# Optimization experiments

Measured on AMD Instinct MI355X. Metric: run time of the kernel, lower is better.

The kernel has to match this reference:

```python
import jax, jax.numpy as jnp
import numpy as np

B, C, O = 16384, 128, 128


def setup_inputs() -> dict:
    key = jax.random.key(0)
    k1, k2, k3 = jax.random.split(key, 3)
    x = jax.random.normal(k1, (B, C, 3, 3), dtype=jnp.float32)
    # 9 stacked Conv2d(C, O, 3x3) weights/biases, position p = 3*r + c (row-major)
    W = jax.random.normal(k2, (9, O, C, 3, 3), dtype=jnp.float32) * 0.05
    b = jax.random.normal(k3, (9, O), dtype=jnp.float32) * 0.05
    return {"x": x, "W": W, "b": b}


def reference(x, W, b):
    Bn = x.shape[0]
    xr = x.reshape(Bn, C, 3, 3)
    # F.interpolate(scale_factor=3, mode='nearest'): each pixel replicated 3x3
    ins = jnp.repeat(jnp.repeat(xr, 3, axis=2), 3, axis=3)  # (B, C, 9, 9)
    # patch for output position (r, c) is ins[:, :, 2+r:5+r, 2+c:5+c]
    patches = jnp.stack(
        [ins[:, :, 2 + r:5 + r, 2 + c:5 + c] for r in range(3) for c in range(3)],
        axis=0,
    )  # (9, B, C, 3, 3)
    # each conv reduces its 3x3xC patch to one pixel per out-channel
    out = jnp.einsum('pbcij,pocij->bpo', patches, W) + b[None]  # (B, 9, O)
    out = out.transpose(0, 2, 1).reshape(Bn, O, 3, 3)  # row-major (r, c)
    return out
```

## Files before the change

kernel.cpp:

```cpp
#include <hip/hip_runtime.h>
#include <hip/hip_bf16.h>

typedef __bf16 bf16_t;
typedef __attribute__((ext_vector_type(8))) __bf16 bf16x8;
typedef __attribute__((ext_vector_type(4))) float f32x4;

#define KDIM 1152
#define NDIM 1152
#define BM 128
#define BN 192
#define BK 32
#define NIT 36
#define NTILES 6
#define A_STEP 8192
#define A_PANEL 294912
#define B_STEP 12288
#define B_TILE (36 * B_STEP)

__device__ __forceinline__ void gload_lds16(const void* g, void* l) {
    __builtin_amdgcn_global_load_lds(
        (const __attribute__((address_space(1))) void*)g,
        (__attribute__((address_space(3))) void*)l, 16, 0, 0);
}

__global__ void cvt_x(const float* __restrict__ X, bf16_t* __restrict__ Xb)
{
    const int u = blockIdx.x * 256 + threadIdx.x;
    const int w = u >> 9;
    const int P = w / 36;
    const int T = w - P * 36;
    const int rem = u & 511;
    const int rb = rem >> 6;
    const int g = (rem >> 4) & 3;
    const int r0 = rem & 15;
    const int m = P * 128 + rb * 16 + r0;
    const int k = T * 32 + g * 8;
    const float* src = X + (size_t)m * KDIM + k;
    f32x4 lo = *(const f32x4*)src;
    f32x4 hi = *(const f32x4*)(src + 4);
    bf16x8 v;
    #pragma unroll
    for (int e = 0; e < 4; ++e) { v[e] = (__bf16)lo[e]; v[4 + e] = (__bf16)hi[e]; }
    *(bf16x8*)((char*)Xb + (size_t)u * 16) = v;
}

__global__ void build_wb(const float* __restrict__ W,
                         const float* __restrict__ bvec,
                         bf16_t* __restrict__ Bm,
                         float* __restrict__ bias)
{
    const int t = blockIdx.x * blockDim.x + threadIdx.x;
    if (t < NDIM) {
        const int o = t / 9, p = t - o * 9;
        bias[t] = bvec[p * 128 + o];
    }
    const int c = t & 127;
    const int o = (t >> 7) & 127;
    const int p = t >> 14;
    if (p >= 9) return;
    const int r = p / 3, cc = p - r * 3;
    float eff[3][3] = {{0.f,0.f,0.f},{0.f,0.f,0.f},{0.f,0.f,0.f}};
    const float* w = W + (size_t)((p * 128 + o) * 128 + c) * 9;
    #pragma unroll
    for (int i = 0; i < 3; ++i) {
        const int a = (2 + r + i) / 3;
        #pragma unroll
        for (int j = 0; j < 3; ++j) {
            const int bb = (2 + cc + j) / 3;
            eff[a][bb] += w[i * 3 + j];
        }
    }
    const int n = o * 9 + p;
    const int tile = n / BN;
    const int nin = n - tile * BN;
    #pragma unroll
    for (int a = 0; a < 3; ++a)
        #pragma unroll
        for (int bb = 0; bb < 3; ++bb) {
            const int k = c * 9 + a * 3 + bb;
            const size_t idx = (size_t)tile * (B_TILE / 2)
                             + (k >> 5) * (B_STEP / 2)
                             + (nin >> 4) * 512 + ((k >> 3) & 3) * 128
                             + (nin & 15) * 8 + (k & 7);
            Bm[idx] = (bf16_t)eff[a][bb];
        }
}

__launch_bounds__(256, 3)
__global__ void ind_gemm(const bf16_t* __restrict__ Xb,
                         const bf16_t* __restrict__ Bm,
                         const float* __restrict__ bias,
                         float* __restrict__ out)
{
    __shared__ char As[2][A_STEP];
    __shared__ char Bs[2][B_STEP];

    const int tid = threadIdx.x;
    const int lane = tid & 63;
    const int wid = tid >> 6;
    const int wm = wid >> 1;
    const int wn = wid & 1;

    const int bid = blockIdx.x;
    const int swz = (bid & 7) * 96 + (bid >> 3);
    const int mt = swz / NTILES;
    const int nt = swz - mt * NTILES;
    const int m0 = mt * BM;

    const char* apanel = (const char*)Xb + (size_t)mt * A_PANEL;
    const char* bpanel = (const char*)Bm + (size_t)nt * B_TILE;
    const int fr = (lane >> 4) * 256 + (lane & 15) * 16;

    f32x4 acc[4][6];
    #pragma unroll
    for (int i = 0; i < 4; ++i)
        #pragma unroll
        for (int j = 0; j < 6; ++j)
            acc[i][j] = (f32x4){0.f, 0.f, 0.f, 0.f};

    #define GLDA(T, BUF) do {                                               \
        const char* s_ = apanel + (size_t)(T) * A_STEP;                     \
        gload_lds16(s_ + tid * 16,        &As[BUF][tid * 16]);              \
        gload_lds16(s_ + 4096 + tid * 16, &As[BUF][4096 + tid * 16]);       \
    } while (0)

    #define GLDB(T, BUF) do {                                               \
        const char* s_ = bpanel + (size_t)(T) * B_STEP;                     \
        _Pragma("unroll")                                                   \
        for (int r_ = 0; r_ < 3; ++r_) {                                    \
            const int u_ = (tid + r_ * 256) * 16;                           \
            gload_lds16(s_ + u_, &Bs[BUF][u_]);                             \
        } } while (0)

    GLDA(0, 0); GLDB(0, 0);
    GLDA(1, 1); GLDB(1, 1);
    asm volatile("s_waitcnt vmcnt(5)" ::: "memory");
    __builtin_amdgcn_sched_barrier(0);
    __builtin_amdgcn_s_barrier();

    #pragma unroll 1
    for (int t = 0; t < NIT; ++t) {
        const int cur = t & 1;
        bf16x8 af[4], bfr[6];
        #pragma unroll
        for (int mi = 0; mi < 4; ++mi)
            af[mi] = *(const bf16x8*)(&As[cur][(wm * 4 + mi) * 1024 + fr]);
        #pragma unroll
        for (int j = 0; j < 6; ++j)
            bfr[j] = *(const bf16x8*)(&Bs[cur][(wn * 6 + j) * 1024 + fr]);
        asm volatile("s_waitcnt lgkmcnt(0)" ::: "memory");
        __builtin_amdgcn_sched_barrier(0);
        __builtin_amdgcn_s_barrier();
        if (t < NIT - 2) {
            GLDA(t + 2, cur);
            GLDB(t + 2, cur);
        }
        __builtin_amdgcn_s_setprio(1);
        #pragma unroll
        for (int mi = 0; mi < 4; ++mi)
            #pragma unroll
            for (int j = 0; j < 6; ++j)
                acc[mi][j] = __builtin_amdgcn_mfma_f32_16x16x32_bf16(
                    af[mi], bfr[j], acc[mi][j], 0, 0, 0);
        __builtin_amdgcn_s_setprio(0);
        if (t < NIT - 2) {
            asm volatile("s_waitcnt vmcnt(5)" ::: "memory");
            __builtin_amdgcn_sched_barrier(0);
        } else if (t == NIT - 2) {
            asm volatile("s_waitcnt vmcnt(0)" ::: "memory");
            __builtin_amdgcn_sched_barrier(0);
        }
        if (t < NIT - 1) __builtin_amdgcn_s_barrier();
    }

    #undef GLDA
    #undef GLDB

    const int orow = (lane >> 4) * 4;
    const int ocol = lane & 15;
    const int gn0 = nt * BN + wn * 96 + ocol;
    #pragma unroll
    for (int ni = 0; ni < 6; ++ni) {
        const float bv = bias[gn0 + ni * 16];
        #pragma unroll
        for (int mi = 0; mi < 4; ++mi) {
            float* po = out + (size_t)(m0 + wm * 64 + mi * 16 + orow) * NDIM
                            + gn0 + ni * 16;
            #pragma unroll
            for (int r = 0; r < 4; ++r)
                po[(size_t)r * NDIM] = acc[mi][ni][r] + bv;
        }
    }
}

extern "C" void kernel_launch(void* const* d_in, const int* in_sizes, int n_in,
                              void* d_out, int out_size, void* d_ws, size_t ws_size,
                              hipStream_t stream)
{
    const float* x  = (const float*)d_in[0];
    const float* W  = (const float*)d_in[1];
    const float* bv = (const float*)d_in[2];
    float* out = (float*)d_out;

    bf16_t* Xb   = (bf16_t*)d_ws;
    bf16_t* Bm   = (bf16_t*)((char*)d_ws + (size_t)16384 * KDIM * sizeof(bf16_t));
    float*  bias = (float*)((char*)Bm + (size_t)KDIM * NDIM * sizeof(bf16_t));

    cvt_x<<<9216, 256, 0, stream>>>(x, Xb);
    build_wb<<<576, 256, 0, stream>>>(W, bv, Bm, bias);
    ind_gemm<<<768, 256, 0, stream>>>(Xb, Bm, bias, out);
}
```

Measured before the change: 89.44 us.

## Load A fragments directly from global into registers, bypassing LDS

The GEMM no longer stages the A panel in shared memory. Each wave loads its A fragments straight into VGPRs with inline-asm global_load_dwordx4, double-buffered in two register sets, and the loop is unrolled by two. Only B is staged through LDS now. This removes the A LDS traffic and its footprint, at the cost of more VGPRs and of duplicated global reads of A by the two wn waves.

```diff
diff --git a/kernel.cpp b/kernel.cpp
--- a/kernel.cpp
+++ b/kernel.cpp
@@ -92,7 +92,6 @@
                          const float* __restrict__ bias,
                          float* __restrict__ out)
 {
-    __shared__ char As[2][A_STEP];
     __shared__ char Bs[2][B_STEP];
 
     const int tid = threadIdx.x;
@@ -107,9 +106,9 @@
     const int nt = swz - mt * NTILES;
     const int m0 = mt * BM;
 
-    const char* apanel = (const char*)Xb + (size_t)mt * A_PANEL;
+    const int fr = (lane >> 4) * 256 + (lane & 15) * 16;
+    const char* apl = (const char*)Xb + (size_t)mt * A_PANEL + wm * 4096 + fr;
     const char* bpanel = (const char*)Bm + (size_t)nt * B_TILE;
-    const int fr = (lane >> 4) * 256 + (lane & 15) * 16;
 
     f32x4 acc[4][6];
     #pragma unroll
@@ -118,10 +117,16 @@
         for (int j = 0; j < 6; ++j)
             acc[i][j] = (f32x4){0.f, 0.f, 0.f, 0.f};
 
-    #define GLDA(T, BUF) do {                                               \
-        const char* s_ = apanel + (size_t)(T) * A_STEP;                     \
-        gload_lds16(s_ + tid * 16,        &As[BUF][tid * 16]);              \
-        gload_lds16(s_ + 4096 + tid * 16, &As[BUF][4096 + tid * 16]);       \
+    f32x4 afA[4], afB[4];
+
+    #define LOADA(T, AF) do {                                               \
+        const char* p_ = apl + (size_t)(T) * A_STEP;                        \
+        asm volatile("global_load_dwordx4 %0, %4, off\n\t"                  \
+                     "global_load_dwordx4 %1, %4, off offset:1024\n\t"      \
+                     "global_load_dwordx4 %2, %4, off offset:2048\n\t"      \
+                     "global_load_dwordx4 %3, %4, off offset:3072"          \
+                     : "=&v"(AF[0]), "=&v"(AF[1]), "=&v"(AF[2]), "=&v"(AF[3]) \
+                     : "v"(p_) : "memory");                                 \
     } while (0)
 
     #define GLDB(T, BUF) do {                                               \
@@ -132,49 +137,74 @@
             gload_lds16(s_ + u_, &Bs[BUF][u_]);                             \
         } } while (0)
 
-    GLDA(0, 0); GLDB(0, 0);
-    GLDA(1, 1); GLDB(1, 1);
-    asm volatile("s_waitcnt vmcnt(5)" ::: "memory");
+    #define MFMA24(AF) do {                                                 \
+        __builtin_amdgcn_s_setprio(1);                                      \
+        _Pragma("unroll")                                                   \
+        for (int mi = 0; mi < 4; ++mi) {                                    \
+            const bf16x8 a_ = __builtin_bit_cast(bf16x8, AF[mi]);           \
+            _Pragma("unroll")                                               \
+            for (int j_ = 0; j_ < 6; ++j_)                                  \
+                acc[mi][j_] = __builtin_amdgcn_mfma_f32_16x16x32_bf16(      \
+                    a_, bfr[j_], acc[mi][j_], 0, 0, 0);                     \
+        }                                                                   \
+        __builtin_amdgcn_s_setprio(0);                                      \
+    } while (0)
+
+    #define RDB(CUR) do {                                                   \
+        _Pragma("unroll")                                                   \
+        for (int j_ = 0; j_ < 6; ++j_)                                      \
+            bfr[j_] = *(const bf16x8*)(&Bs[CUR][(wn * 6 + j_) * 1024 + fr]); \
+        asm volatile("s_waitcnt lgkmcnt(0)" ::: "memory");                  \
+        __builtin_amdgcn_sched_barrier(0);                                  \
+        __builtin_amdgcn_s_barrier();                                       \
+    } while (0)
+
+    bf16x8 bfr[6];
+
+    LOADA(0, afA);
+    GLDB(0, 0);
+    GLDB(1, 1);
+    asm volatile("s_waitcnt vmcnt(3)" ::: "memory");
     __builtin_amdgcn_sched_barrier(0);
     __builtin_amdgcn_s_barrier();
 
     #pragma unroll 1
-    for (int t = 0; t < NIT; ++t) {
-        const int cur = t & 1;
-        bf16x8 af[4], bfr[6];
-        #pragma unroll
-        for (int mi = 0; mi < 4; ++mi)
-            af[mi] = *(const bf16x8*)(&As[cur][(wm * 4 + mi) * 1024 + fr]);
-        #pragma unroll
-        for (int j = 0; j < 6; ++j)
-            bfr[j] = *(const bf16x8*)(&Bs[cur][(wn * 6 + j) * 1024 + fr]);
+    for (int t2 = 0; t2 < 17; ++t2) {
+        const int t = 2 * t2;
+        RDB(0);
+        LOADA(t + 1, afB);
+        GLDB(t + 2, 0);
+        MFMA24(afA);
+        asm volatile("s_waitcnt vmcnt(3)" ::: "memory");
+        __builtin_amdgcn_sched_barrier(0);
+        __builtin_amdgcn_s_barrier();
+        RDB(1);
+        LOADA(t + 2, afA);
+        GLDB(t + 3, 1);
+        MFMA24(afB);
+        asm volatile("s_waitcnt vmcnt(3)" ::: "memory");
+        __builtin_amdgcn_sched_barrier(0);
+        __builtin_amdgcn_s_barrier();
+    }
+    RDB(0);
+    LOADA(35, afB);
+    MFMA24(afA);
+    asm volatile("s_waitcnt vmcnt(0)" ::: "memory");
+    __builtin_amdgcn_sched_barrier(0);
+    __builtin_amdgcn_s_barrier();
+    {
+        #pragma unroll
+        for (int j_ = 0; j_ < 6; ++j_)
+            bfr[j_] = *(const bf16x8*)(&Bs[1][(wn * 6 + j_) * 1024 + fr]);
         asm volatile("s_waitcnt lgkmcnt(0)" ::: "memory");
         __builtin_amdgcn_sched_barrier(0);
-        __builtin_amdgcn_s_barrier();
-        if (t < NIT - 2) {
-            GLDA(t + 2, cur);
-            GLDB(t + 2, cur);
-        }
-        __builtin_amdgcn_s_setprio(1);
-        #pragma unroll
-        for (int mi = 0; mi < 4; ++mi)
-            #pragma unroll
-            for (int j = 0; j < 6; ++j)
-                acc[mi][j] = __builtin_amdgcn_mfma_f32_16x16x32_bf16(
-                    af[mi], bfr[j], acc[mi][j], 0, 0, 0);
-        __builtin_amdgcn_s_setprio(0);
-        if (t < NIT - 2) {
-            asm volatile("s_waitcnt vmcnt(5)" ::: "memory");
-            __builtin_amdgcn_sched_barrier(0);
-        } else if (t == NIT - 2) {
-            asm volatile("s_waitcnt vmcnt(0)" ::: "memory");
-            __builtin_amdgcn_sched_barrier(0);
-        }
-        if (t < NIT - 1) __builtin_amdgcn_s_barrier();
-    }
-
-    #undef GLDA
+        MFMA24(afB);
+    }
+
+    #undef LOADA
     #undef GLDB
+    #undef MFMA24
+    #undef RDB
 
     const int orow = (lane >> 4) * 4;
     const int ocol = lane & 15;
```

Measured after the change: 90.53 us. Within noise of the previous version (+1.2%).

## Enlarge GEMM tiles to 256x288 with 512-thread blocks and 4-slot LDS ring

Applied to the files above, without the earlier changes.

The bf16 GEMM tile grows from 128x192 with 256 threads to 256x288 with 512 threads. The grid shrinks to 256 blocks, one per CU. Each block stages A and B into a 4-slot LDS ring, prefetching two steps ahead, and splits each K-step into two half-steps so global-to-LDS loads interleave with MFMA work. The aim is more data reuse per loaded byte and less global and L2 traffic. In exchange there are fewer resident waves per CU, higher register pressure from 36 accumulators per wave, and a scrap LDS write to keep the per-thread load count uniform.

```diff
diff --git a/kernel.cpp b/kernel.cpp
--- a/kernel.cpp
+++ b/kernel.cpp
@@ -7,15 +7,13 @@
 
 #define KDIM 1152
 #define NDIM 1152
-#define BM 128
-#define BN 192
-#define BK 32
-#define NIT 36
-#define NTILES 6
-#define A_STEP 8192
+#define BM 256
+#define BN 288
+#define NH 36
+#define NTILES 4
 #define A_PANEL 294912
-#define B_STEP 12288
-#define B_TILE (36 * B_STEP)
+#define B_SLAB 18432
+#define B_TILE (36 * B_SLAB)
 
 __device__ __forceinline__ void gload_lds16(const void* g, void* l) {
     __builtin_amdgcn_global_load_lds(
@@ -79,21 +77,22 @@
         for (int bb = 0; bb < 3; ++bb) {
             const int k = c * 9 + a * 3 + bb;
             const size_t idx = (size_t)tile * (B_TILE / 2)
-                             + (k >> 5) * (B_STEP / 2)
+                             + (k >> 5) * (B_SLAB / 2)
                              + (nin >> 4) * 512 + ((k >> 3) & 3) * 128
                              + (nin & 15) * 8 + (k & 7);
             Bm[idx] = (bf16_t)eff[a][bb];
         }
 }
 
-__launch_bounds__(256, 3)
+__launch_bounds__(512, 1)
 __global__ void ind_gemm(const bf16_t* __restrict__ Xb,
                          const bf16_t* __restrict__ Bm,
                          const float* __restrict__ bias,
                          float* __restrict__ out)
 {
-    __shared__ char As[2][A_STEP];
-    __shared__ char Bs[2][B_STEP];
+    __shared__ char Ar[4][16384];
+    __shared__ char Br[4][18432];
+    __shared__ char Scrap[1024];
 
     const int tid = threadIdx.x;
     const int lane = tid & 63;
@@ -102,85 +101,113 @@
     const int wn = wid & 1;
 
     const int bid = blockIdx.x;
-    const int swz = (bid & 7) * 96 + (bid >> 3);
-    const int mt = swz / NTILES;
-    const int nt = swz - mt * NTILES;
+    const int swz = (bid & 7) * 32 + (bid >> 3);
+    const int mt = swz >> 2;
+    const int nt = swz & 3;
     const int m0 = mt * BM;
 
-    const char* apanel = (const char*)Xb + (size_t)mt * A_PANEL;
-    const char* bpanel = (const char*)Bm + (size_t)nt * B_TILE;
+    const char* apan0 = (const char*)Xb + (size_t)(2 * mt) * A_PANEL;
+    const char* apan1 = apan0 + A_PANEL;
+    const char* bpan  = (const char*)Bm + (size_t)nt * B_TILE;
+
     const int fr = (lane >> 4) * 256 + (lane & 15) * 16;
-
-    f32x4 acc[4][6];
+    const int aoff = (wm >> 1) * 8192 + (wm & 1) * 4096;
+
+    f32x4 acc[4][9];
     #pragma unroll
     for (int i = 0; i < 4; ++i)
         #pragma unroll
-        for (int j = 0; j < 6; ++j)
+        for (int j = 0; j < 9; ++j)
             acc[i][j] = (f32x4){0.f, 0.f, 0.f, 0.f};
 
-    #define GLDA(T, BUF) do {                                               \
-        const char* s_ = apanel + (size_t)(T) * A_STEP;                     \
-        gload_lds16(s_ + tid * 16,        &As[BUF][tid * 16]);              \
-        gload_lds16(s_ + 4096 + tid * 16, &As[BUF][4096 + tid * 16]);       \
+    bf16x8 af0, af1, af2, af3, bfr[9];
+
+    #define STAGE_A0(H) gload_lds16(apan0 + (size_t)(H) * 8192 + tid * 16,  \
+                                    &Ar[(H) & 3][tid * 16])
+    #define STAGE_A1(H) gload_lds16(apan1 + (size_t)(H) * 8192 + tid * 16,  \
+                                    &Ar[(H) & 3][8192 + tid * 16])
+    #define STAGE_B0(H) gload_lds16(bpan + (size_t)(H) * B_SLAB + tid * 16, \
+                                    &Br[(H) & 3][tid * 16])
+    #define STAGE_B1(H) gload_lds16(bpan + (size_t)(H) * B_SLAB + (tid + 512) * 16, \
+                                    &Br[(H) & 3][(tid + 512) * 16])
+    #define STAGE_B2(H) do {                                                \
+        if (tid < 128)                       \
+            gload_lds16(bpan + (size_t)(H) * B_SLAB + (tid + 1024) * 16,    \
+                        &Br[(H) & 3][(tid + 1024) * 16]);                   \
+        else                     \
+            gload_lds16(bpan + tid * 16, Scrap);                            \
     } while (0)
 
-    #define GLDB(T, BUF) do {                                               \
-        const char* s_ = bpanel + (size_t)(T) * B_STEP;                     \
+    #define LDB(S) do {                                                     \
         _Pragma("unroll")                                                   \
-        for (int r_ = 0; r_ < 3; ++r_) {                                    \
-            const int u_ = (tid + r_ * 256) * 16;                           \
-            gload_lds16(s_ + u_, &Bs[BUF][u_]);                             \
-        } } while (0)
-
-    GLDA(0, 0); GLDB(0, 0);
-    GLDA(1, 1); GLDB(1, 1);
+        for (int j_ = 0; j_ < 9; ++j_)                                      \
+            bfr[j_] = *(const bf16x8*)(&Br[S][(wn * 9 + j_) * 1024 + fr]);  \
+    } while (0)
+
+    #define LDA(DST, S, MI)                                                 \
+        DST = *(const bf16x8*)(&Ar[S][aoff + (MI) * 1024 + fr])
+
+    #define MM(AF, MI) do {                                                 \
+        _Pragma("unroll")                                                   \
+        for (int j_ = 0; j_ < 9; ++j_)                                      \
+            acc[MI][j_] = __builtin_amdgcn_mfma_f32_16x16x32_bf16(          \
+                AF, bfr[j_], acc[MI][j_], 0, 0, 0);                         \
+    } while (0)
+
+    #define BAR()   __builtin_amdgcn_s_barrier()
+    #define LGKM0() do { asm volatile("s_waitcnt lgkmcnt(0)" ::: "memory"); \
+                         __builtin_amdgcn_sched_barrier(0); } while (0)
+
+    STAGE_A0(0); STAGE_A1(0); STAGE_B0(0); STAGE_B1(0); STAGE_B2(0);
+    STAGE_A0(1); STAGE_A1(1); STAGE_B0(1); STAGE_B1(1); STAGE_B2(1);
     asm volatile("s_waitcnt vmcnt(5)" ::: "memory");
     __builtin_amdgcn_sched_barrier(0);
-    __builtin_amdgcn_s_barrier();
+    BAR();
 
     #pragma unroll 1
-    for (int t = 0; t < NIT; ++t) {
-        const int cur = t & 1;
-        bf16x8 af[4], bfr[6];
-        #pragma unroll
-        for (int mi = 0; mi < 4; ++mi)
-            af[mi] = *(const bf16x8*)(&As[cur][(wm * 4 + mi) * 1024 + fr]);
-        #pragma unroll
-        for (int j = 0; j < 6; ++j)
-            bfr[j] = *(const bf16x8*)(&Bs[cur][(wn * 6 + j) * 1024 + fr]);
-        asm volatile("s_waitcnt lgkmcnt(0)" ::: "memory");
-        __builtin_amdgcn_sched_barrier(0);
-        __builtin_amdgcn_s_barrier();
-        if (t < NIT - 2) {
-            GLDA(t + 2, cur);
-            GLDB(t + 2, cur);
-        }
+    for (int h = 0; h < NH; ++h) {
+        const int s = h & 3;
+        const bool st = (h <= NH - 3);
+        LDB(s);
+        LDA(af0, s, 0); LDA(af1, s, 1);
+        if (st) { STAGE_A0(h + 2); STAGE_B0(h + 2); }
+        BAR(); LGKM0();
         __builtin_amdgcn_s_setprio(1);
-        #pragma unroll
-        for (int mi = 0; mi < 4; ++mi)
-            #pragma unroll
-            for (int j = 0; j < 6; ++j)
-                acc[mi][j] = __builtin_amdgcn_mfma_f32_16x16x32_bf16(
-                    af[mi], bfr[j], acc[mi][j], 0, 0, 0);
+        MM(af0, 0); MM(af1, 1);
         __builtin_amdgcn_s_setprio(0);
-        if (t < NIT - 2) {
+        BAR();
+        LDA(af2, s, 2); LDA(af3, s, 3);
+        if (st) { STAGE_A1(h + 2); STAGE_B1(h + 2); STAGE_B2(h + 2); }
+        BAR(); LGKM0();
+        __builtin_amdgcn_s_setprio(1);
+        MM(af2, 2); MM(af3, 3);
+        __builtin_amdgcn_s_setprio(0);
+        if (h <= NH - 3) {
             asm volatile("s_waitcnt vmcnt(5)" ::: "memory");
             __builtin_amdgcn_sched_barrier(0);
-        } else if (t == NIT - 2) {
+        } else if (h == NH - 2) {
             asm volatile("s_waitcnt vmcnt(0)" ::: "memory");
             __builtin_amdgcn_sched_barrier(0);
         }
-        if (t < NIT - 1) __builtin_amdgcn_s_barrier();
-    }
-
-    #undef GLDA
-    #undef GLDB
+        BAR();
+    }
+
+    #undef STAGE_A0
+    #undef STAGE_A1
+    #undef STAGE_B0
+    #undef STAGE_B1
+    #undef STAGE_B2
+    #undef LDB
+    #undef LDA
+    #undef MM
+    #undef BAR
+    #undef LGKM0
 
     const int orow = (lane >> 4) * 4;
     const int ocol = lane & 15;
-    const int gn0 = nt * BN + wn * 96 + ocol;
-    #pragma unroll
-    for (int ni = 0; ni < 6; ++ni) {
+    const int gn0 = nt * BN + wn * 144 + ocol;
+    #pragma unroll
+    for (int ni = 0; ni < 9; ++ni) {
         const float bv = bias[gn0 + ni * 16];
         #pragma unroll
         for (int mi = 0; mi < 4; ++mi) {
@@ -208,5 +235,5 @@
 
     cvt_x<<<9216, 256, 0, stream>>>(x, Xb);
     build_wb<<<576, 256, 0, stream>>>(W, bv, Bm, bias);
-    ind_gemm<<<768, 256, 0, stream>>>(Xb, Bm, bias, out);
-}
+    ind_gemm<<<256, 512, 0, stream>>>(Xb, Bm, bias, out);
+}
```

Result: slower. 94.97 us (+6.2%).
